# Optimization experiments

Hardware: AMD Instinct MI355X
Metric: run time of the kernel (lower is better)

## Reference

```python
import jax, jax.numpy as jnp
import numpy as np

EPS = 1e-6


def setup_inputs() -> dict:
    key = jax.random.key(0)
    k_x, k_qkv, k_proj = jax.random.split(key, 3)
    B, C, H, W, D = 4, 256, 16, 16, 16
    x = jax.random.normal(k_x, (B, C, H, W, D), dtype=jnp.float32)
    # 1x1 Conv3d == per-position linear; init roughly like torch conv default
    fan_in = C
    bound = 1.0 / np.sqrt(fan_in)
    qkv_w = jax.random.uniform(k_qkv, (3 * C, C), jnp.float32, -bound, bound)
    qkv_b = jnp.zeros((3 * C,), jnp.float32)
    proj_w = jax.random.uniform(k_proj, (C, C), jnp.float32, -bound, bound)
    proj_b = jnp.zeros((C,), jnp.float32)
    norm_gamma = jnp.ones((C,), jnp.float32)
    norm_beta = jnp.zeros((C,), jnp.float32)
    return {"x": x, "norm_gamma": norm_gamma, "norm_beta": norm_beta,
            "qkv_w": qkv_w, "qkv_b": qkv_b, "proj_w": proj_w, "proj_b": proj_b}


def reference(x, norm_gamma, norm_beta, qkv_w, qkv_b, proj_w, proj_b):
    B, C, H, W, D = x.shape
    N = H * W * D
    scale = float(C) ** -0.5

    # GroupNorm with num_groups=1: normalize over (C,H,W,D) per sample (biased var)
    mean = jnp.mean(x, axis=(1, 2, 3, 4), keepdims=True)
    var = jnp.mean(jnp.square(x - mean), axis=(1, 2, 3, 4), keepdims=True)
    xn = (x - mean) * jax.lax.rsqrt(var + EPS)
    xn = xn * norm_gamma[None, :, None, None, None] + norm_beta[None, :, None, None, None]

    xn_flat = xn.reshape(B, C, N)  # b c n
    # 1x1 conv == channel-mixing GEMM
    qkv = jnp.einsum('oc,bcn->bon', qkv_w, xn_flat) + qkv_b[None, :, None]  # [B, 3C, N]
    q, k, v = jnp.split(qkv, 3, axis=1)  # each [B, C, N]

    w = jnp.einsum('bcq,bck->bqk', q, k) * scale  # [B, N, N]
    w = jax.nn.softmax(w, axis=-1)
    h = jnp.einsum('bqk,bck->bcq', w, v)  # [B, C, N]

    h = jnp.einsum('oc,bcn->bon', proj_w, h) + proj_b[None, :, None]
    return x + h.reshape(B, C, H, W, D)
```

## Files before the change

### kernel.cpp

```cpp
#include <hip/hip_runtime.h>

typedef __attribute__((ext_vector_type(8))) short short8;
typedef __attribute__((ext_vector_type(4))) float f32x4;
typedef __attribute__((ext_vector_type(16))) float f32x16;
typedef __attribute__((ext_vector_type(4))) int i32x4;

__device__ __forceinline__ unsigned short f2bf(float f){
  union { float f; unsigned int u; } cv; cv.f = f;
  unsigned int u = cv.u;
  u = (u + 0x7fffu + ((u >> 16) & 1u)) >> 16;
  return (unsigned short)u;
}
__device__ __forceinline__ float bf2f(unsigned short h){
  union { unsigned int u; float f; } cv; cv.u = ((unsigned int)h) << 16;
  return cv.f;
}

typedef unsigned int u32g __attribute__((address_space(1)));
typedef unsigned int u32l __attribute__((address_space(3)));
__device__ __forceinline__ void gload16(const void* g, void* l){
  __builtin_amdgcn_global_load_lds((const u32g*)g, (u32l*)l, 16, 0, 0);
}

__device__ __forceinline__ unsigned int cvtpk_bf16(float lo, float hi){
  unsigned int r;
  asm("v_cvt_pk_bf16_f32 %0, %1, %2" : "=v"(r) : "v"(lo), "v"(hi));
  return r;
}
__device__ __forceinline__ unsigned int cvt2_fp8(float a, float b){
  unsigned int r;
  asm("v_cvt_pk_fp8_f32 %0, %1, %2" : "=v"(r) : "v"(a), "v"(b));
  return r;
}

#define BARRIER() asm volatile("s_barrier" ::: "memory")
#define WAITV(N)  asm volatile("s_waitcnt vmcnt(" #N ")" ::: "memory")
#define WAITLGKM0() asm volatile("s_waitcnt lgkmcnt(0)" ::: "memory")

__global__ __launch_bounds__(256) void fused_pre_k(const float* __restrict__ x,
                                                   float2* __restrict__ partial,
                                                   const float* __restrict__ qkv_w,
                                                   const float* __restrict__ qkv_b,
                                                   const float* __restrict__ proj_w,
                                                   unsigned short* __restrict__ Wqk,
                                                   unsigned short* __restrict__ Wv,
                                                   unsigned short* __restrict__ Wp,
                                                   float* __restrict__ bias_qk){
  const int blk = blockIdx.x;
  if (blk < 256){
    const int b = blk >> 6, xb = blk & 63;
    const float4* xp = (const float4*)(x + (size_t)b*1048576 + (size_t)xb*16384);
    float s = 0.f, sq = 0.f;
    #pragma unroll
    for (int i = 0; i < 16; ++i){
      float4 v = xp[threadIdx.x + i*256];
      s  += v.x + v.y + v.z + v.w;
      sq += v.x*v.x + v.y*v.y + v.z*v.z + v.w*v.w;
    }
    #pragma unroll
    for (int m = 1; m < 64; m <<= 1){ s += __shfl_xor(s, m); sq += __shfl_xor(sq, m); }
    __shared__ float2 acc[4];
    if ((threadIdx.x & 63) == 0) acc[threadIdx.x >> 6] = make_float2(s, sq);
    __syncthreads();
    if (threadIdx.x == 0){
      float S = 0.f, Q = 0.f;
      for (int i = 0; i < 4; ++i){ S += acc[i].x; Q += acc[i].y; }
      partial[b*64 + xb] = make_float2(S, Q);
    }
  } else {
    int id = (blk - 256) * 256 + threadIdx.x;
    if (id < 131072){
      Wqk[id] = f2bf(qkv_w[id]);
      if (id < 512) bias_qk[id] = qkv_b[id];
    } else if (id < 196608){
      Wv[id - 131072] = f2bf(qkv_w[id]);
    } else {
      int j = id - 196608;
      Wp[j] = f2bf(proj_w[j]);
    }
  }
}

__global__ __launch_bounds__(256) void norm_transpose_k(const float* __restrict__ x,
                                                        const float* __restrict__ gamma,
                                                        const float* __restrict__ beta,
                                                        const float2* __restrict__ partial,
                                                        unsigned short* __restrict__ xnt){
  __shared__ float tile[64][65];
  __shared__ float2 stt;
  const int b = blockIdx.z, n0 = blockIdx.x*64, c0 = blockIdx.y*64;
  const int t = threadIdx.x;
  if (t < 64){
    float2 p = partial[b*64 + t];
    float s = p.x, q = p.y;
    #pragma unroll
    for (int m = 1; m < 64; m <<= 1){ s += __shfl_xor(s, m); q += __shfl_xor(q, m); }
    if (t == 0){
      const float inv = 1.0f/1048576.0f;
      float mean = s*inv;
      float var  = q*inv - mean*mean;
      stt = make_float2(mean, rsqrtf(var + 1e-6f));
    }
  }
  __syncthreads();
  const float2 st = stt;
  const int col = t & 63, rb = t >> 6;
  #pragma unroll
  for (int i = 0; i < 16; ++i){
    int rr = i*4 + rb;
    float xv = x[((size_t)b*256 + c0 + rr)*4096 + n0 + col];
    tile[rr][col] = (xv - st.x) * st.y * gamma[c0+rr] + beta[c0+rr];
  }
  __syncthreads();
  #pragma unroll
  for (int i = 0; i < 16; ++i){
    int nr = i*4 + rb;
    xnt[((size_t)b*4096 + n0 + nr)*256 + c0 + col] = f2bf(tile[col][nr]);
  }
}

__global__ __launch_bounds__(256) void gemm_nt_k(const unsigned short* __restrict__ A,
                                                 const unsigned short* __restrict__ B,
                                                 int lda, int ldb, long sA, long sB,
                                                 const float* __restrict__ bias_m,
                                                 const float* __restrict__ bias_n,
                                                 const float* __restrict__ resid, long sR,
                                                 float* __restrict__ outF,
                                                 unsigned short* __restrict__ outB,
                                                 unsigned char* __restrict__ out8,
                                                 int ldc, long sC, int vtile){
  __shared__ unsigned short As[64][40];
  __shared__ unsigned short Bs[64][40];
  const int b  = blockIdx.z;
  const int m0 = blockIdx.x * 64, n0 = blockIdx.y * 64;
  const unsigned short* Ab = A + (size_t)b * sA;
  const unsigned short* Bb = B + (size_t)b * sB;
  const int t = threadIdx.x;
  const int lane = t & 63, w = t >> 6;
  const int g = lane >> 4, r = lane & 15;
  const int wm = (w >> 1) * 32, wn = (w & 1) * 32;
  const int lrow = t >> 2, lcol = (t & 3) * 8;
  f32x4 acc00 = {0,0,0,0}, acc01 = {0,0,0,0}, acc10 = {0,0,0,0}, acc11 = {0,0,0,0};
  for (int ks = 0; ks < 8; ++ks){
    short8 av = *(const short8*)(Ab + (size_t)(m0 + lrow) * lda + ks*32 + lcol);
    short8 bv = *(const short8*)(Bb + (size_t)(n0 + lrow) * ldb + ks*32 + lcol);
    __syncthreads();
    *(short8*)&As[lrow][lcol] = av;
    *(short8*)&Bs[lrow][lcol] = bv;
    __syncthreads();
    short8 af0 = *(const short8*)&As[wm + r][g*8];
    short8 af1 = *(const short8*)&As[wm + 16 + r][g*8];
    short8 bf0 = *(const short8*)&Bs[wn + r][g*8];
    short8 bf1 = *(const short8*)&Bs[wn + 16 + r][g*8];
    acc00 = __builtin_amdgcn_mfma_f32_16x16x32_bf16(af0, bf0, acc00, 0, 0, 0);
    acc01 = __builtin_amdgcn_mfma_f32_16x16x32_bf16(af0, bf1, acc01, 0, 0, 0);
    acc10 = __builtin_amdgcn_mfma_f32_16x16x32_bf16(af1, bf0, acc10, 0, 0, 0);
    acc11 = __builtin_amdgcn_mfma_f32_16x16x32_bf16(af1, bf1, acc11, 0, 0, 0);
  }
  f32x4 accs[2][2] = {{acc00, acc01},{acc10, acc11}};
  #pragma unroll
  for (int mi = 0; mi < 2; ++mi)
    #pragma unroll
    for (int ni = 0; ni < 2; ++ni)
      #pragma unroll
      for (int j = 0; j < 4; ++j){
        int gm = m0 + wm + mi*16 + g*4 + j;
        int gn = n0 + wn + ni*16 + r;
        float vv = accs[mi][ni][j];
        if (bias_m) vv += bias_m[gm];
        if (bias_n) vv += bias_n[gn];
        if (resid)  vv += resid[(size_t)b*sR + (size_t)gm*ldc + gn];
        if (out8){
          out8[(size_t)b*sC + (size_t)gm*ldc + gn] = (unsigned char)(cvt2_fp8(vv, vv) & 0xff);
        } else if (outB){
          size_t off;
          if (vtile)
            off = (size_t)b*sC + (size_t)(gn >> 4)*4096 + (size_t)(gm >> 5)*512
                + ((gn >> 3) & 1)*256 + (gm & 31)*8 + (gn & 7);
          else
            off = (size_t)b*sC + (size_t)gm*ldc + gn;
          outB[off] = f2bf(vv);
        } else {
          outF[(size_t)b*sC + (size_t)gm*ldc + gn] = vv;
        }
      }
}

__global__ __launch_bounds__(256, 2) void attn_k(const unsigned char* __restrict__ qk8,
                                                 const unsigned short* __restrict__ vt,
                                                 unsigned short* __restrict__ po,
                                                 float* __restrict__ ml){
  __shared__ __align__(16) char smem[49152];
  const int id = blockIdx.x;
  const int combo = id & 15, qb = id >> 4;
  const int b = combo >> 2, ks = combo & 3;
  const int q0 = qb * 128;
  const int t = threadIdx.x, lane = t & 63, w = t >> 6;
  const int hi = lane >> 5, l31 = lane & 31;
  const unsigned char* qkb = qk8 + (size_t)b * 4096 * 512;
  const unsigned short* vtb = vt + (size_t)b * 1048576;
  const float SQL2 = 0.0625f * 1.44269504088896340736f;

  unsigned long long qf[16];
  {
    const unsigned char* qrow = qkb + (size_t)(q0 + w*32 + l31) * 512;
    #pragma unroll
    for (int s = 0; s < 16; ++s) qf[s] = *(const unsigned long long*)(qrow + s*16 + hi*8);
  }

  auto stageK = [&](int kt, char* buf){
    const int kbase = ks*1024 + kt*32;
    #pragma unroll
    for (int i2 = 0; i2 < 2; ++i2){
      int ci = (w*2 + i2)*64 + lane;
      int r = ci >> 4;
      const unsigned char* src = qkb + (size_t)(kbase + r)*512 + 256
                               + (((ci & 15) ^ (r & 15)) * 16);
      gload16(src, buf + (w*2 + i2)*1024);
    }
  };
  auto stageV = [&](int kt, char* buf){
    const int kbase = ks*1024 + kt*32;
    #pragma unroll
    for (int i = 0; i < 4; ++i){
      int tix = w*4 + i;
      const unsigned short* src = vtb + (size_t)((kbase >> 4) + (tix >> 3))*4096
                                + (tix & 7)*512 + lane*8;
      gload16(src, buf + 8192 + tix*1024);
    }
  };
  stageK(0, smem);
  stageV(0, smem);

  f32x16 O[8];
  #pragma unroll
  for (int cb = 0; cb < 8; ++cb)
    #pragma unroll
    for (int jj = 0; jj < 16; ++jj) O[cb][jj] = 0.f;
  float lrun = 0.f;
  const int ksw = (l31 & 15) << 4;

  for (int kt = 0; kt < 32; ++kt){
    char* cur = smem + (kt & 1)*24576;
    char* nxt = smem + ((kt + 1) & 1)*24576;

    WAITV(0);
    BARRIER();

    int ktn = (kt < 31) ? kt + 1 : 31;
    stageK(ktn, nxt);
    stageV(ktn, nxt);

    f32x16 Sa, Sb;
    #pragma unroll
    for (int jj = 0; jj < 16; ++jj){ Sa[jj] = 0.f; Sb[jj] = 0.f; }
    const char* kp = cur + l31*256;
    __builtin_amdgcn_s_setprio(1);
    #pragma unroll
    for (int s = 0; s < 8; ++s){
      unsigned long long k0 = *(const unsigned long long*)(kp + (((2*s  )*16 + hi*8) ^ ksw));
      unsigned long long k1 = *(const unsigned long long*)(kp + (((2*s+1)*16 + hi*8) ^ ksw));
      Sa = __builtin_amdgcn_mfma_f32_32x32x16_fp8_fp8((long long)k0, (long long)qf[2*s  ], Sa, 0, 0, 0);
      Sb = __builtin_amdgcn_mfma_f32_32x32x16_fp8_fp8((long long)k1, (long long)qf[2*s+1], Sb, 0, 0, 0);
    }
    __builtin_amdgcn_s_setprio(0);

    float p[16];
    #pragma unroll
    for (int jj = 0; jj < 16; ++jj)
      p[jj] = __builtin_amdgcn_exp2f(fmaf(Sa[jj] + Sb[jj], SQL2, -24.0f));
    lrun += ((p[0]+p[1]) + (p[2]+p[3])) + ((p[4]+p[5]) + (p[6]+p[7]))
          + ((p[8]+p[9]) + (p[10]+p[11])) + ((p[12]+p[13]) + (p[14]+p[15]));
    unsigned int a0 = cvtpk_bf16(p[0],p[1]),   a1 = cvtpk_bf16(p[2],p[3]);
    unsigned int a2 = cvtpk_bf16(p[4],p[5]),   a3 = cvtpk_bf16(p[6],p[7]);
    unsigned int a4 = cvtpk_bf16(p[8],p[9]),   a5 = cvtpk_bf16(p[10],p[11]);
    unsigned int a6 = cvtpk_bf16(p[12],p[13]), a7 = cvtpk_bf16(p[14],p[15]);
    asm("v_permlane32_swap_b32 %0, %1" : "+v"(a0), "+v"(a2));
    asm("v_permlane32_swap_b32 %0, %1" : "+v"(a1), "+v"(a3));
    asm("v_permlane32_swap_b32 %0, %1" : "+v"(a4), "+v"(a6));
    asm("v_permlane32_swap_b32 %0, %1" : "+v"(a5), "+v"(a7));
    i32x4 u0 = {(int)a0,(int)a1,(int)a2,(int)a3};
    i32x4 u1 = {(int)a4,(int)a5,(int)a6,(int)a7};
    short8 pa0 = __builtin_bit_cast(short8, u0);
    short8 pa1 = __builtin_bit_cast(short8, u1);

    const char* Vt = cur + 8192;
    __builtin_amdgcn_s_setprio(1);
    #pragma unroll
    for (int cb = 0; cb < 8; ++cb){
      short8 v0 = *(const short8*)(Vt + (0*8 + cb)*1024 + lane*16);
      O[cb] = __builtin_amdgcn_mfma_f32_32x32x16_bf16(v0, pa0, O[cb], 0, 0, 0);
      short8 v1 = *(const short8*)(Vt + (1*8 + cb)*1024 + lane*16);
      O[cb] = __builtin_amdgcn_mfma_f32_32x32x16_bf16(v1, pa1, O[cb], 0, 0, 0);
    }
    __builtin_amdgcn_s_setprio(0);
  }
  WAITV(0);

  float lf = lrun + __shfl_xor(lrun, 32);
  const int qg = q0 + w*32 + l31;
  unsigned short* pob = po + (size_t)combo * 1048576;
  #pragma unroll
  for (int cb = 0; cb < 8; ++cb)
    #pragma unroll
    for (int jj = 0; jj < 16; ++jj){
      int c = cb*32 + (jj & 3) + 8*(jj >> 2) + 4*hi;
      pob[(size_t)c*4096 + qg] = f2bf(O[cb][jj]);
    }
  if (lane < 32)
    ml[(size_t)combo*4096 + qg] = lf;
}

__global__ __launch_bounds__(256) void attn_merge_k(const unsigned short* __restrict__ po,
                                                    const float* __restrict__ ml,
                                                    unsigned short* __restrict__ ho){
  __shared__ float Of[64][261];
  const int b = blockIdx.y, q0 = blockIdx.x * 64;
  const int t = threadIdx.x, ql = t & 63, ci = t >> 6;
  const int q = q0 + ql;
  float L = 0.f;
  #pragma unroll
  for (int ksv = 0; ksv < 4; ++ksv)
    L += ml[(size_t)(b*4 + ksv)*4096 + q];
  float inv = 1.0f / L;
  float acc[64];
  #pragma unroll
  for (int i = 0; i < 64; ++i) acc[i] = 0.f;
  #pragma unroll
  for (int ksv = 0; ksv < 4; ++ksv){
    const unsigned short* pb = po + (size_t)(b*4 + ksv)*1048576 + q;
    #pragma unroll
    for (int i = 0; i < 64; ++i)
      acc[i] += bf2f(pb[(size_t)(ci + 4*i)*4096]);
  }
  #pragma unroll
  for (int i = 0; i < 64; ++i) Of[ql][ci + 4*i] = acc[i] * inv;
  __syncthreads();
  const int qr = t >> 2, sub = t & 3;
  const float* rowp = Of[qr];
  unsigned short* dst = ho + ((size_t)(b*4096 + q0 + qr))*256;
  #pragma unroll
  for (int jj = 0; jj < 8; ++jj){
    int c = sub*8 + jj*32;
    float4 v0 = *(const float4*)(rowp + c);
    float4 v1 = *(const float4*)(rowp + c + 4);
    short8 o;
    o[0] = (short)f2bf(v0.x); o[1] = (short)f2bf(v0.y);
    o[2] = (short)f2bf(v0.z); o[3] = (short)f2bf(v0.w);
    o[4] = (short)f2bf(v1.x); o[5] = (short)f2bf(v1.y);
    o[6] = (short)f2bf(v1.z); o[7] = (short)f2bf(v1.w);
    *(short8*)(dst + c) = o;
  }
}

extern "C" void kernel_launch(void* const* d_in, const int* in_sizes, int n_in,
                              void* d_out, int out_size, void* d_ws, size_t ws_size,
                              hipStream_t stream){
  const float* x      = (const float*)d_in[0];
  const float* gamma  = (const float*)d_in[1];
  const float* beta   = (const float*)d_in[2];
  const float* qkv_w  = (const float*)d_in[3];
  const float* qkv_b  = (const float*)d_in[4];
  const float* proj_w = (const float*)d_in[5];
  const float* proj_b = (const float*)d_in[6];
  float* out = (float*)d_out;
  char* ws = (char*)d_ws;

  float2* partial        = (float2*)(ws + 0);
  float*  bias_qk        = (float*)(ws + 4096);
  unsigned short* Wqk    = (unsigned short*)(ws + 8192);
  unsigned short* Wv     = (unsigned short*)(ws + 270336);
  unsigned short* Wp     = (unsigned short*)(ws + 401408);
  unsigned short* xnt    = (unsigned short*)(ws + 532480);
  unsigned char*  qk8    = (unsigned char*)(ws + 8921088);
  unsigned short* vt     = (unsigned short*)(ws + 17309696);
  unsigned short* po     = (unsigned short*)(ws + 25698304);
  float*          ml     = (float*)(ws + 59252736);
  unsigned short* ho     = xnt;

  fused_pre_k<<<1280, 256, 0, stream>>>(x, partial, qkv_w, qkv_b, proj_w,
                                        Wqk, Wv, Wp, bias_qk);
  norm_transpose_k<<<dim3(64,4,4), 256, 0, stream>>>(x, gamma, beta, partial, xnt);
  gemm_nt_k<<<dim3(64,8,4), 256, 0, stream>>>(xnt, Wqk, 256, 256, 4096L*256, 0,
      nullptr, bias_qk, nullptr, 0, nullptr, nullptr, qk8, 512, 4096L*512, 0);
  gemm_nt_k<<<dim3(4,64,4), 256, 0, stream>>>(Wv, xnt, 256, 256, 0, 4096L*256,
      qkv_b + 512, nullptr, nullptr, 0, nullptr, vt, nullptr, 4096, 256L*4096, 1);
  attn_k<<<dim3(512), 256, 0, stream>>>(qk8, vt, po, ml);
  attn_merge_k<<<dim3(64,4), 256, 0, stream>>>(po, ml, ho);
  gemm_nt_k<<<dim3(4,64,4), 256, 0, stream>>>(Wp, ho, 256, 256, 0, 4096L*256,
      proj_b, nullptr, x, 1048576L, out, nullptr, nullptr, 4096, 1048576L, 0);
}
```

Before: 138.1 us.

## Store V and softmax probabilities in FP8 and run PV product with FP8 MFMA

The V projection now writes FP8 in a swizzled tiled layout instead of BF16. The attention kernel stages half as many V bytes into a smaller LDS buffer, converts probabilities to packed FP8 and uses the FP8 32x32x16 MFMA for the P·V product. This cuts V global traffic, LDS footprint and MFMA cost. In exchange it loses precision in both P and V, and it drops the -24 exponent offset, so unnormalized probabilities now sit near 1 rather than being scaled down before the FP8 conversion.

```diff
diff --git a/kernel.cpp b/kernel.cpp
--- a/kernel.cpp
+++ b/kernel.cpp
@@ -22,11 +22,6 @@
   __builtin_amdgcn_global_load_lds((const u32g*)g, (u32l*)l, 16, 0, 0);
 }
 
-__device__ __forceinline__ unsigned int cvtpk_bf16(float lo, float hi){
-  unsigned int r;
-  asm("v_cvt_pk_bf16_f32 %0, %1, %2" : "=v"(r) : "v"(lo), "v"(hi));
-  return r;
-}
 __device__ __forceinline__ unsigned int cvt2_fp8(float a, float b){
   unsigned int r;
   asm("v_cvt_pk_fp8_f32 %0, %1, %2" : "=v"(r) : "v"(a), "v"(b));
@@ -171,15 +166,16 @@
         if (bias_n) vv += bias_n[gn];
         if (resid)  vv += resid[(size_t)b*sR + (size_t)gm*ldc + gn];
         if (out8){
-          out8[(size_t)b*sC + (size_t)gm*ldc + gn] = (unsigned char)(cvt2_fp8(vv, vv) & 0xff);
+          size_t off;
+          if (vtile == 2){
+            int inner = ((gm & 31)*16 + (gn & 15)) ^ (((gm >> 3) & 1) << 3);
+            off = (size_t)b*sC + (size_t)((gn >> 4)*8 + (gm >> 5))*512 + inner;
+          } else {
+            off = (size_t)b*sC + (size_t)gm*ldc + gn;
+          }
+          out8[off] = (unsigned char)(cvt2_fp8(vv, vv) & 0xff);
         } else if (outB){
-          size_t off;
-          if (vtile)
-            off = (size_t)b*sC + (size_t)(gn >> 4)*4096 + (size_t)(gm >> 5)*512
-                + ((gn >> 3) & 1)*256 + (gm & 31)*8 + (gn & 7);
-          else
-            off = (size_t)b*sC + (size_t)gm*ldc + gn;
-          outB[off] = f2bf(vv);
+          outB[(size_t)b*sC + (size_t)gm*ldc + gn] = f2bf(vv);
         } else {
           outF[(size_t)b*sC + (size_t)gm*ldc + gn] = vv;
         }
@@ -187,10 +183,10 @@
 }
 
 __global__ __launch_bounds__(256, 2) void attn_k(const unsigned char* __restrict__ qk8,
-                                                 const unsigned short* __restrict__ vt,
+                                                 const unsigned char* __restrict__ vt8,
                                                  unsigned short* __restrict__ po,
                                                  float* __restrict__ ml){
-  __shared__ __align__(16) char smem[49152];
+  __shared__ __align__(16) char smem[32768];
   const int id = blockIdx.x;
   const int combo = id & 15, qb = id >> 4;
   const int b = combo >> 2, ks = combo & 3;
@@ -198,7 +194,7 @@
   const int t = threadIdx.x, lane = t & 63, w = t >> 6;
   const int hi = lane >> 5, l31 = lane & 31;
   const unsigned char* qkb = qk8 + (size_t)b * 4096 * 512;
-  const unsigned short* vtb = vt + (size_t)b * 1048576;
+  const unsigned char* vtb = vt8 + (size_t)b * 1048576;
   const float SQL2 = 0.0625f * 1.44269504088896340736f;
 
   unsigned long long qf[16];
@@ -222,11 +218,12 @@
   auto stageV = [&](int kt, char* buf){
     const int kbase = ks*1024 + kt*32;
     #pragma unroll
-    for (int i = 0; i < 4; ++i){
-      int tix = w*4 + i;
-      const unsigned short* src = vtb + (size_t)((kbase >> 4) + (tix >> 3))*4096
-                                + (tix & 7)*512 + lane*8;
-      gload16(src, buf + 8192 + tix*1024);
+    for (int i = 0; i < 2; ++i){
+      int tp = (w*2 + i)*2;
+      int tile = tp + (lane >> 5);
+      const unsigned char* src = vtb + (size_t)((kbase >> 4) + (tile >> 3))*4096
+                               + (tile & 7)*512 + (lane & 31)*16;
+      gload16(src, buf + 8192 + tp*512);
     }
   };
   stageK(0, smem);
@@ -239,10 +236,12 @@
     for (int jj = 0; jj < 16; ++jj) O[cb][jj] = 0.f;
   float lrun = 0.f;
   const int ksw = (l31 & 15) << 4;
+  const int vsw = ((l31 >> 3) & 1) << 3;
+  const int vbase = l31*16 + hi*8;
 
   for (int kt = 0; kt < 32; ++kt){
-    char* cur = smem + (kt & 1)*24576;
-    char* nxt = smem + ((kt + 1) & 1)*24576;
+    char* cur = smem + (kt & 1)*16384;
+    char* nxt = smem + ((kt + 1) & 1)*16384;
 
     WAITV(0);
     BARRIER();
@@ -268,30 +267,30 @@
     float p[16];
     #pragma unroll
     for (int jj = 0; jj < 16; ++jj)
-      p[jj] = __builtin_amdgcn_exp2f(fmaf(Sa[jj] + Sb[jj], SQL2, -24.0f));
+      p[jj] = __builtin_amdgcn_exp2f((Sa[jj] + Sb[jj]) * SQL2);
     lrun += ((p[0]+p[1]) + (p[2]+p[3])) + ((p[4]+p[5]) + (p[6]+p[7]))
           + ((p[8]+p[9]) + (p[10]+p[11])) + ((p[12]+p[13]) + (p[14]+p[15]));
-    unsigned int a0 = cvtpk_bf16(p[0],p[1]),   a1 = cvtpk_bf16(p[2],p[3]);
-    unsigned int a2 = cvtpk_bf16(p[4],p[5]),   a3 = cvtpk_bf16(p[6],p[7]);
-    unsigned int a4 = cvtpk_bf16(p[8],p[9]),   a5 = cvtpk_bf16(p[10],p[11]);
-    unsigned int a6 = cvtpk_bf16(p[12],p[13]), a7 = cvtpk_bf16(p[14],p[15]);
-    asm("v_permlane32_swap_b32 %0, %1" : "+v"(a0), "+v"(a2));
-    asm("v_permlane32_swap_b32 %0, %1" : "+v"(a1), "+v"(a3));
-    asm("v_permlane32_swap_b32 %0, %1" : "+v"(a4), "+v"(a6));
-    asm("v_permlane32_swap_b32 %0, %1" : "+v"(a5), "+v"(a7));
-    i32x4 u0 = {(int)a0,(int)a1,(int)a2,(int)a3};
-    i32x4 u1 = {(int)a4,(int)a5,(int)a6,(int)a7};
-    short8 pa0 = __builtin_bit_cast(short8, u0);
-    short8 pa1 = __builtin_bit_cast(short8, u1);
+    unsigned A0 = (unsigned)__builtin_amdgcn_cvt_pk_fp8_f32(p[0],  p[1],  0, false);
+    A0 = (unsigned)__builtin_amdgcn_cvt_pk_fp8_f32(p[2],  p[3],  (int)A0, true);
+    unsigned B0 = (unsigned)__builtin_amdgcn_cvt_pk_fp8_f32(p[4],  p[5],  0, false);
+    B0 = (unsigned)__builtin_amdgcn_cvt_pk_fp8_f32(p[6],  p[7],  (int)B0, true);
+    unsigned A1 = (unsigned)__builtin_amdgcn_cvt_pk_fp8_f32(p[8],  p[9],  0, false);
+    A1 = (unsigned)__builtin_amdgcn_cvt_pk_fp8_f32(p[10], p[11], (int)A1, true);
+    unsigned B1 = (unsigned)__builtin_amdgcn_cvt_pk_fp8_f32(p[12], p[13], 0, false);
+    B1 = (unsigned)__builtin_amdgcn_cvt_pk_fp8_f32(p[14], p[15], (int)B1, true);
+    asm("v_permlane32_swap_b32 %0, %1" : "+v"(A0), "+v"(B0));
+    asm("v_permlane32_swap_b32 %0, %1" : "+v"(A1), "+v"(B1));
+    long long pb0 = (long long)(((unsigned long long)B0 << 32) | A0);
+    long long pb1 = (long long)(((unsigned long long)B1 << 32) | A1);
 
     const char* Vt = cur + 8192;
     __builtin_amdgcn_s_setprio(1);
     #pragma unroll
     for (int cb = 0; cb < 8; ++cb){
-      short8 v0 = *(const short8*)(Vt + (0*8 + cb)*1024 + lane*16);
-      O[cb] = __builtin_amdgcn_mfma_f32_32x32x16_bf16(v0, pa0, O[cb], 0, 0, 0);
-      short8 v1 = *(const short8*)(Vt + (1*8 + cb)*1024 + lane*16);
-      O[cb] = __builtin_amdgcn_mfma_f32_32x32x16_bf16(v1, pa1, O[cb], 0, 0, 0);
+      unsigned long long v0 = *(const unsigned long long*)(Vt + (0*8 + cb)*512 + (vbase ^ vsw));
+      O[cb] = __builtin_amdgcn_mfma_f32_32x32x16_fp8_fp8((long long)v0, pb0, O[cb], 0, 0, 0);
+      unsigned long long v1 = *(const unsigned long long*)(Vt + (1*8 + cb)*512 + (vbase ^ vsw));
+      O[cb] = __builtin_amdgcn_mfma_f32_32x32x16_fp8_fp8((long long)v1, pb1, O[cb], 0, 0, 0);
     }
     __builtin_amdgcn_s_setprio(0);
   }
@@ -373,7 +372,7 @@
   unsigned short* Wp     = (unsigned short*)(ws + 401408);
   unsigned short* xnt    = (unsigned short*)(ws + 532480);
   unsigned char*  qk8    = (unsigned char*)(ws + 8921088);
-  unsigned short* vt     = (unsigned short*)(ws + 17309696);
+  unsigned char*  vt8    = (unsigned char*)(ws + 17309696);
   unsigned short* po     = (unsigned short*)(ws + 25698304);
   float*          ml     = (float*)(ws + 59252736);
   unsigned short* ho     = xnt;
@@ -384,8 +383,8 @@
   gemm_nt_k<<<dim3(64,8,4), 256, 0, stream>>>(xnt, Wqk, 256, 256, 4096L*256, 0,
       nullptr, bias_qk, nullptr, 0, nullptr, nullptr, qk8, 512, 4096L*512, 0);
   gemm_nt_k<<<dim3(4,64,4), 256, 0, stream>>>(Wv, xnt, 256, 256, 0, 4096L*256,
-      qkv_b + 512, nullptr, nullptr, 0, nullptr, vt, nullptr, 4096, 256L*4096, 1);
-  attn_k<<<dim3(512), 256, 0, stream>>>(qk8, vt, po, ml);
+      qkv_b + 512, nullptr, nullptr, 0, nullptr, nullptr, vt8, 4096, 1048576L, 2);
+  attn_k<<<dim3(512), 256, 0, stream>>>(qk8, vt8, po, ml);
   attn_merge_k<<<dim3(64,4), 256, 0, stream>>>(po, ml, ho);
   gemm_nt_k<<<dim3(4,64,4), 256, 0, stream>>>(Wp, ho, 256, 256, 0, 4096L*256,
       proj_b, nullptr, x, 1048576L, out, nullptr, nullptr, 4096, 1048576L, 0);
```

Result: faster. 128.9 us (-6.7%).
